# Kernel optimization log

Measured on AMD Instinct MI355X. Metric: run time of the kernel, lower is better.

The kernel has to match this reference:

```python
import jax, jax.numpy as jnp
import numpy as np
import math


def _forward(x, f0, theta, sigma, theta0, fbs, mix, w1, b1, w2, b2, conv_w):
    B, I, H, W = x.shape          # config requires B == I == H (== W here)
    S, O, _ = f0.shape            # config requires O == 1
    # ---- log-Gabor filter bank, fully vectorized over (scale, out, in) ----
    yy = jnp.linspace(-1.0, 1.0, H)[:, None]   # meshgrid 'ij': y along rows
    xx = jnp.linspace(-1.0, 1.0, W)[None, :]
    r = jnp.sqrt(xx ** 2 + yy ** 2 + 1e-6)     # [H,W]
    phi = jnp.arctan2(yy, xx)                  # [H,W]
    lr = jnp.log(r)
    log_gabor = jnp.exp(-(lr - jnp.log(f0)[..., None, None]) ** 2
                        / (2.0 * jnp.log(sigma)[..., None, None] ** 2))
    angular = jnp.exp(-(phi - theta[..., None, None]) ** 2
                      / (2.0 * theta0[..., None, None] ** 2))
    filters = log_gabor * angular              # [S,O,I,H,W]
    # ---- FFT (torch fftshift default shifts ALL dims; jnp matches) ----
    xs = jnp.fft.fftshift(jnp.fft.fft2(x))     # [B,I,H,W] complex64
    # ---- frequency attention (two 1x1 convs + softmax over scales) ----
    h1 = jax.nn.relu(jnp.einsum('bchw,oc->bohw', jnp.abs(xs), w1)
                     + b1[None, :, None, None])
    aw = jax.nn.softmax(jnp.einsum('bchw,sc->bshw', h1, w2)
                        + b2[None, :, None, None], axis=1)   # [B,S,H,W]
    # ---- attention-weighted combine. Faithful to torch broadcasting with
    # O==1 and B==I: attended[0,b,i,h,w] = sum_s xs[b,i]*F[s,0,i]*aw[i,s] ----
    attended = jnp.einsum('bihw,sihw,ishw->bihw', xs, filters[:, 0], aw)[None]
    # ---- dynamic frequency band mask (torch slices dims 2,3 = (Cin,H)) ----
    s_idx = jnp.floor((fbs[0, :, 0] + 1.0) / 2.0 * H).astype(jnp.int32)  # [I]
    e_idx = jnp.floor((fbs[0, :, 1] + 1.0) / 2.0 * H).astype(jnp.int32)
    arI = jnp.arange(I)
    arH = jnp.arange(H)
    mk = (arI[None, :] >= s_idx[:, None]) & (arI[None, :] < e_idx[:, None])  # [J,I]
    mh = (arH[None, :] >= s_idx[:, None]) & (arH[None, :] < e_idx[:, None])  # [J,H]
    mask = (mk[:, :, None] & mh[:, None, :]).astype(x.dtype)                 # [J,I,H]
    attended = attended * mask[None, :, :, :, None]
    # ---- back to spatial domain ----
    x_filtered = jnp.fft.ifft2(jnp.fft.ifftshift(attended)).real  # [1,B,I,H,W]
    # ---- spatial 3x3 conv path ----
    x_spatial = jax.lax.conv_general_dilated(
        x, conv_w, window_strides=(1, 1), padding=((1, 1), (1, 1)),
        dimension_numbers=('NCHW', 'OIHW', 'NCHW'))               # [B,1,H,W]
    return mix * x_filtered + (1.0 - mix) * x_spatial[None]


def setup_inputs() -> dict:
    key = jax.random.key(0)
    ks = jax.random.split(key, 10)
    B = I = H = W = 64
    O, S, HID = 1, 3, 64
    PI = math.pi
    x = jax.random.normal(ks[0], (B, I, H, W), dtype=jnp.float32)
    f0 = jnp.ones((S, O, I), jnp.float32)
    theta0 = jnp.ones((S, O, I), jnp.float32)
    sigma = jax.random.uniform(ks[1], (S, O, I), jnp.float32) * PI
    theta = jax.random.uniform(ks[2], (S, O, I), jnp.float32) * PI
    fbs = jax.random.uniform(ks[3], (O, I, 2), jnp.float32)
    mix = jax.random.uniform(ks[4], (1,), jnp.float32)
    w1 = jax.random.normal(ks[5], (HID, I), jnp.float32) * 0.05
    b1 = jnp.zeros((HID,), jnp.float32)
    w2 = jax.random.normal(ks[6], (S, HID), jnp.float32) * 0.05
    b2 = jnp.zeros((S,), jnp.float32)
    conv_w = jax.random.normal(ks[7], (O, I, 3, 3), jnp.float32) / math.sqrt(I * 9)
    return {'x': x, 'f0': f0, 'theta': theta, 'sigma': sigma, 'theta0': theta0,
            'fbs': fbs, 'mix': mix, 'w1': w1, 'b1': b1, 'w2': w2, 'b2': b2,
            'conv_w': conv_w}


def reference(x, f0, theta, sigma, theta0, fbs, mix, w1, b1, w2, b2, conv_w):
    return _forward(x, f0, theta, sigma, theta0, fbs, mix, w1, b1, w2, b2, conv_w)
```

## Files before the change

kernel.cpp:

```cpp
#include <hip/hip_runtime.h>

#define PI_D 3.14159265358979323846

namespace {
constexpr float CT[33] = {
  1.0000000000f,  0.9951847267f,  0.9807852804f,  0.9569403357f,
  0.9238795325f,  0.8819212643f,  0.8314696123f,  0.7730104534f,
  0.7071067812f,  0.6343932842f,  0.5555702330f,  0.4713967368f,
  0.3826834324f,  0.2902846773f,  0.1950903220f,  0.0980171403f,
  0.0f,          -0.0980171403f, -0.1950903220f, -0.2902846773f,
 -0.3826834324f, -0.4713967368f, -0.5555702330f, -0.6343932842f,
 -0.7071067812f, -0.7730104534f, -0.8314696123f, -0.8819212643f,
 -0.9238795325f, -0.9569403357f, -0.9807852804f, -0.9951847267f,
 -1.0f};
constexpr float STb[33] = {
  0.0f,           0.0980171403f,  0.1950903220f,  0.2902846773f,
  0.3826834324f,  0.4713967368f,  0.5555702330f,  0.6343932842f,
  0.7071067812f,  0.7730104534f,  0.8314696123f,  0.8819212643f,
  0.9238795325f,  0.9569403357f,  0.9807852804f,  0.9951847267f,
  1.0f,           0.9951847267f,  0.9807852804f,  0.9569403357f,
  0.9238795325f,  0.8819212643f,  0.8314696123f,  0.7730104534f,
  0.7071067812f,  0.6343932842f,  0.5555702330f,  0.4713967368f,
  0.3826834324f,  0.2902846773f,  0.1950903220f,  0.0980171403f,
  0.0f};
}

__device__ __forceinline__ void bitrev64(float v[64]) {
#pragma unroll
  for (int i = 0; i < 64; ++i) {
    const int j = (int)(__brev((unsigned)i) >> 26);
    if (j > i) { const float tv = v[i]; v[i] = v[j]; v[j] = tv; }
  }
}

template <bool INV, bool REAL>
__device__ __forceinline__ void fft64_stages(float re[64], float im[64]) {
#pragma unroll
  for (int s = 0; s < 6; ++s) {
    const int half = 1 << s;
    const int m = half << 1;
    const int tstep = 32 >> s;
#pragma unroll
    for (int k = 0; k < 64; k += m) {
#pragma unroll
      for (int j = 0; j < half; ++j) {
        const int ti = j * tstep;
        const int a = k + j, b = k + j + half;
        if (REAL && j == 0) {
          const float tr = re[b];
          re[b] = re[a] - tr;
          re[a] = re[a] + tr;
        } else if (REAL && ti == 16) {
          const float t0 = re[b];
          re[b] = re[a];
          im[b] = t0;
          im[a] = -t0;
        } else {
          float tr, tii;
          if (ti == 0) {
            tr = re[b]; tii = im[b];
          } else if (ti == 16) {
            if (INV) { tr = -im[b]; tii = re[b]; }
            else     { tr =  im[b]; tii = -re[b]; }
          } else {
            const float wr = CT[ti];
            const float wi = INV ? STb[ti] : -STb[ti];
            tr  = re[b] * wr - im[b] * wi;
            tii = re[b] * wi + im[b] * wr;
          }
          re[b] = re[a] - tr;  im[b] = im[a] - tii;
          re[a] = re[a] + tr;  im[a] = im[a] + tii;
        }
      }
    }
  }
}

template <bool INV>
__device__ __forceinline__ void fft64_regs(float re[64], float im[64]) {
  bitrev64(re);
  bitrev64(im);
  fft64_stages<INV, false>(re, im);
}

__device__ __forceinline__ void fft64_fwd_real(float re[64], float im[64]) {
  bitrev64(re);
  fft64_stages<false, true>(re, im);
}

__device__ __forceinline__ void band_from_fbs(const float* __restrict__ fbs,
                                              int c, int& s0, int& e0) {
  s0 = (int)floorf((fbs[2 * c]     + 1.0f) * 0.5f * 64.0f);
  e0 = (int)floorf((fbs[2 * c + 1] + 1.0f) * 0.5f * 64.0f);
}

__global__ __launch_bounds__(64) void k_fft_fwd(const float* __restrict__ x,
                                                float* __restrict__ F,
                                                const float* __restrict__ fbs,
                                                const float* __restrict__ w1,
                                                float* __restrict__ w1T) {
  __shared__ float buf[64][65];
  const int t = threadIdx.x;
  const int img = blockIdx.x;
  if (img == 0) {
    for (int k = 0; k < 64; ++k) w1T[t * 64 + k] = w1[k * 64 + t];
  }
  const float* xp = x + ((size_t)img << 12);
  const float4* xr4 = reinterpret_cast<const float4*>(xp + (t << 6));
  float re[64], im[64];
#pragma unroll
  for (int q = 0; q < 16; ++q) {
    const float4 v = xr4[q];
    re[4 * q]     = v.x; re[4 * q + 1] = v.y;
    re[4 * q + 2] = v.z; re[4 * q + 3] = v.w;
  }
#pragma unroll
  for (int j = 0; j < 64; ++j) im[j] = 0.0f;
  fft64_fwd_real(re, im);
#pragma unroll
  for (int j = 0; j < 64; ++j) buf[t][j] = re[j];
  __syncthreads();
#pragma unroll
  for (int j = 0; j < 64; ++j) re[j] = buf[j][t];
  __syncthreads();
#pragma unroll
  for (int j = 0; j < 64; ++j) buf[t][j] = im[j];
  __syncthreads();
#pragma unroll
  for (int j = 0; j < 64; ++j) im[j] = buf[j][t];
  fft64_regs<false>(re, im);
  const int b = img >> 6, i = img & 63;
  const int b_s = (b + 32) & 63, i_s = (i + 32) & 63;
  int s0, e0;
  band_from_fbs(fbs, b_s, s0, e0);
  float* Fre = F + ((size_t)img << 13);
  if ((i_s >= s0) && (i_s < e0)) {
    float* Fim = Fre + 4096;
#pragma unroll
    for (int j = 0; j < 64; ++j) {
      Fre[j * 64 + t] = re[j];
      Fim[j * 64 + t] = im[j];
    }
  } else {
#pragma unroll
    for (int j = 0; j < 64; ++j)
      Fre[j * 64 + t] = sqrtf(re[j] * re[j] + im[j] * im[j]);
  }
}

__global__ __launch_bounds__(64, 4) void k_attn_conv(
    const float* __restrict__ F, const float* __restrict__ w1T,
    const float* __restrict__ b1, const float* __restrict__ w2,
    const float* __restrict__ b2, const float* __restrict__ f0,
    const float* __restrict__ theta, const float* __restrict__ sigma,
    const float* __restrict__ theta0, const float* __restrict__ fbs,
    float* __restrict__ Wc,
    const float* __restrict__ x, const float* __restrict__ cw,
    const float* __restrict__ mixp, float* __restrict__ xsp,
    float* __restrict__ out) {
  const int t = threadIdx.x;
  const unsigned blk = blockIdx.x;
  const unsigned id = blk >> 1;

  if (blk & 1u) {
    const int lane = t;
    const int b = (int)(id >> 6);
    const int row = (int)(id & 63u);
    const float* xb = x + ((size_t)b << 18);
    const int rm = row > 0 ? row - 1 : 0;
    const int rp = row < 63 ? row + 1 : 63;
    float P00 = 0.f, P01 = 0.f, P02 = 0.f;
    float P10 = 0.f, P11 = 0.f, P12 = 0.f;
    float P20 = 0.f, P21 = 0.f, P22 = 0.f;
#pragma unroll 4
    for (int ch = 0; ch < 64; ++ch) {
      const float* xc = xb + (ch << 12);
      const float v0 = xc[(rm << 6) + lane];
      const float v1 = xc[(row << 6) + lane];
      const float v2 = xc[(rp << 6) + lane];
      const float* wp = cw + ch * 9;
      P00 = fmaf(v0, wp[0], P00);
      P01 = fmaf(v0, wp[1], P01);
      P02 = fmaf(v0, wp[2], P02);
      P10 = fmaf(v1, wp[3], P10);
      P11 = fmaf(v1, wp[4], P11);
      P12 = fmaf(v1, wp[5], P12);
      P20 = fmaf(v2, wp[6], P20);
      P21 = fmaf(v2, wp[7], P21);
      P22 = fmaf(v2, wp[8], P22);
    }
    const float tmask = (row > 0) ? 1.0f : 0.0f;
    const float bmask = (row < 63) ? 1.0f : 0.0f;
    const float Ql = tmask * P00 + P10 + bmask * P20;
    const float Qm = tmask * P01 + P11 + bmask * P21;
    const float Qr = tmask * P02 + P12 + bmask * P22;
    const float fromL = __shfl_up(Ql, 1, 64);
    const float fromR = __shfl_down(Qr, 1, 64);
    float acc = Qm;
    if (lane > 0) acc += fromL;
    if (lane < 63) acc += fromR;
    xsp[((size_t)b << 12) + (row << 6) + lane] = acc;
    const int b_s = (b + 32) & 63;
    int s0, e0;
    band_from_fbs(fbs, b_s, s0, e0);
    const float val = (1.0f - mixp[0]) * acc;
    float* ob = out + ((size_t)b << 18) + (row << 6) + lane;
#pragma unroll 4
    for (int i2 = 0; i2 < 64; ++i2) {
      const int i_s = (i2 + 32) & 63;
      if (!(i_s >= s0 && i_s < e0)) ob[(size_t)i2 << 12] = val;
    }
    return;
  }

  const int ai = (int)id;
  const int lane = t;
  const int i = ai >> 6;
  const int h = ai & 63;
  const int b_f = (i + 32) & 63;
  const int u_f = (h + 32) & 63;
  const int v_f = (lane + 32) & 63;
  const int pos_f = (u_f << 6) + v_f;
  int s0a, e0a;
  band_from_fbs(fbs, i, s0a, e0a);
  int alo = s0a < 0 ? 0 : (s0a > 64 ? 64 : s0a);
  int ahi = e0a < 0 ? 0 : (e0a > 64 ? 64 : e0a);
  if (ahi < alo) ahi = alo;
  float acc[64];
#pragma unroll
  for (int k = 0; k < 64; ++k) acc[k] = 0.0f;
  const float* Fb = F + ((size_t)(b_f << 6) << 13) + pos_f;
#pragma unroll 4
  for (int c = 0; c < alo; ++c) {
    const int c_f = (c + 32) & 63;
    const float mc = Fb[(size_t)c_f << 13];
    const float* wrow = w1T + (c << 6);
#pragma unroll
    for (int k = 0; k < 64; ++k) acc[k] = fmaf(wrow[k], mc, acc[k]);
  }
#pragma unroll 2
  for (int c = alo; c < ahi; ++c) {
    const int c_f = (c + 32) & 63;
    const float* base = Fb + ((size_t)c_f << 13);
    const float xr = base[0], xi = base[4096];
    const float mc = sqrtf(xr * xr + xi * xi);
    const float* wrow = w1T + (c << 6);
#pragma unroll
    for (int k = 0; k < 64; ++k) acc[k] = fmaf(wrow[k], mc, acc[k]);
  }
#pragma unroll 4
  for (int c = ahi; c < 64; ++c) {
    const int c_f = (c + 32) & 63;
    const float mc = Fb[(size_t)c_f << 13];
    const float* wrow = w1T + (c << 6);
#pragma unroll
    for (int k = 0; k < 64; ++k) acc[k] = fmaf(wrow[k], mc, acc[k]);
  }
  float l0 = b2[0], l1 = b2[1], l2 = b2[2];
#pragma unroll
  for (int k = 0; k < 64; ++k) {
    const float hv = fmaxf(acc[k] + b1[k], 0.0f);
    l0 = fmaf(w2[k], hv, l0);
    l1 = fmaf(w2[64 + k], hv, l1);
    l2 = fmaf(w2[128 + k], hv, l2);
  }
  float mx = fmaxf(l0, fmaxf(l1, l2));
  float e0v = expf(l0 - mx), e1 = expf(l1 - mx), e2 = expf(l2 - mx);
  float inv = 1.0f / (e0v + e1 + e2);
  float aw0 = e0v * inv, aw1 = e1 * inv, aw2 = e2 * inv;
  const float yy = -1.0f + (float)h * (2.0f / 63.0f);
  const float xx = -1.0f + (float)lane * (2.0f / 63.0f);
  const float r = sqrtf(xx * xx + yy * yy + 1e-6f);
  const float lr = logf(r);
  const float phi = atan2f(yy, xx);
  float wc = 0.0f;
  const float aws[3] = {aw0, aw1, aw2};
#pragma unroll
  for (int s = 0; s < 3; ++s) {
    const float f0v = f0[s * 64 + i];
    const float sgv = sigma[s * 64 + i];
    const float thv = theta[s * 64 + i];
    const float t0v = theta0[s * 64 + i];
    const float ls = logf(sgv);
    const float d1 = lr - logf(f0v);
    const float g1 = expf(-(d1 * d1) / (2.0f * ls * ls));
    const float d2 = phi - thv;
    const float g2 = expf(-(d2 * d2) / (2.0f * t0v * t0v));
    wc = fmaf(g1 * g2, aws[s], wc);
  }
  Wc[((i << 6) + h) * 64 + lane] = wc;
}

__global__ __launch_bounds__(64) void k_ifft_act(
    const float* __restrict__ F, const float* __restrict__ Wc,
    const float* __restrict__ xsp, const float* __restrict__ fbs,
    const float* __restrict__ mixp, float* __restrict__ out) {
  const int img = blockIdx.x;
  const int b = img >> 6, i = img & 63;
  const int b_s = (b + 32) & 63, i_s = (i + 32) & 63;
  int s0, e0;
  band_from_fbs(fbs, b_s, s0, e0);
  if (!((i_s >= s0) && (i_s < e0))) return;
  __shared__ float buf[64][65];
  const int t = threadIdx.x;
  const float* Fre = F + ((size_t)img << 13);
  const float* Fim = Fre + 4096;
  const float* Wcp = Wc + ((size_t)i_s << 12);
  const int u_s = (t + 32) & 63;
  const float rmask = (u_s >= s0 && u_s < e0) ? 1.0f : 0.0f;
  const float* wrow = Wcp + (u_s << 6);
  const float4* fr4 = reinterpret_cast<const float4*>(Fre + (t << 6));
  const float4* fi4 = reinterpret_cast<const float4*>(Fim + (t << 6));
  float re[64], im[64];
#pragma unroll
  for (int q = 0; q < 16; ++q) {
    const int j0 = 4 * q;
    const float4 w4 = *reinterpret_cast<const float4*>(wrow + ((j0 + 32) & 63));
    const float4 vr = fr4[q];
    const float4 vi = fi4[q];
    const float w0 = rmask * w4.x, w1v = rmask * w4.y;
    const float w2v = rmask * w4.z, w3v = rmask * w4.w;
    re[j0]     = vr.x * w0;  re[j0 + 1] = vr.y * w1v;
    re[j0 + 2] = vr.z * w2v; re[j0 + 3] = vr.w * w3v;
    im[j0]     = vi.x * w0;  im[j0 + 1] = vi.y * w1v;
    im[j0 + 2] = vi.z * w2v; im[j0 + 3] = vi.w * w3v;
  }
  fft64_regs<true>(re, im);
#pragma unroll
  for (int j = 0; j < 64; ++j) buf[t][j] = re[j];
  __syncthreads();
#pragma unroll
  for (int j = 0; j < 64; ++j) re[j] = buf[j][t];
  __syncthreads();
#pragma unroll
  for (int j = 0; j < 64; ++j) buf[t][j] = im[j];
  __syncthreads();
#pragma unroll
  for (int j = 0; j < 64; ++j) im[j] = buf[j][t];
  fft64_regs<true>(re, im);
  const float mixv = mixp[0];
  const float sc = mixv * (1.0f / 4096.0f);
  const float om = 1.0f - mixv;
  float* op = out + ((size_t)img << 12);
  const float* xp = xsp + ((size_t)b << 12);
#pragma unroll
  for (int j = 0; j < 64; ++j)
    op[j * 64 + t] = fmaf(sc, re[j], om * xp[j * 64 + t]);
}

extern "C" void kernel_launch(void* const* d_in, const int* in_sizes, int n_in,
                              void* d_out, int out_size, void* d_ws, size_t ws_size,
                              hipStream_t stream) {
  const float* x      = (const float*)d_in[0];
  const float* f0     = (const float*)d_in[1];
  const float* theta  = (const float*)d_in[2];
  const float* sigma  = (const float*)d_in[3];
  const float* theta0 = (const float*)d_in[4];
  const float* fbs    = (const float*)d_in[5];
  const float* mix    = (const float*)d_in[6];
  const float* w1     = (const float*)d_in[7];
  const float* b1     = (const float*)d_in[8];
  const float* w2     = (const float*)d_in[9];
  const float* b2     = (const float*)d_in[10];
  const float* cw     = (const float*)d_in[11];
  float* out = (float*)d_out;
  char* ws = (char*)d_ws;
  float* F   = (float*)(ws);
  float* Wc  = (float*)(ws + 134217728);
  float* xsp = (float*)(ws + 134217728 + 1048576);
  float* w1T = (float*)(ws + 134217728 + 2097152);

  k_fft_fwd<<<4096, 64, 0, stream>>>(x, F, fbs, w1, w1T);
  k_attn_conv<<<8192, 64, 0, stream>>>(F, w1T, b1, w2, b2, f0, theta, sigma,
                                       theta0, fbs, Wc, x, cw, mix, xsp, out);
  k_ifft_act<<<4096, 64, 0, stream>>>(F, Wc, xsp, fbs, mix, out);
}
```

Measured before the change: 234.0 us.

## Split attention hidden dimension across four waves with LDS reduction

The attention blocks grow to 256 threads, and each of the four waves computes 16 of the 64 hidden units. Partial logits are then reduced through shared memory, which cuts per-thread accumulator registers from 64 to 16 and should raise occupancy. The conv path now packs four rows per block, using a 4:1 block interleave instead of alternating blocks. The cost is a block barrier and redundant reads of F by all four waves, plus three idle waves after the reduction.

```diff
diff --git a/kernel.cpp b/kernel.cpp
--- a/kernel.cpp
+++ b/kernel.cpp
@@ -148,7 +148,7 @@
   }
 }
 
-__global__ __launch_bounds__(64, 4) void k_attn_conv(
+__global__ __launch_bounds__(256, 4) void k_attn_conv(
     const float* __restrict__ F, const float* __restrict__ w1T,
     const float* __restrict__ b1, const float* __restrict__ w2,
     const float* __restrict__ b2, const float* __restrict__ f0,
@@ -158,14 +158,17 @@
     const float* __restrict__ x, const float* __restrict__ cw,
     const float* __restrict__ mixp, float* __restrict__ xsp,
     float* __restrict__ out) {
+  __shared__ float part[4][3][64];
   const int t = threadIdx.x;
   const unsigned blk = blockIdx.x;
-  const unsigned id = blk >> 1;
-
-  if (blk & 1u) {
-    const int lane = t;
-    const int b = (int)(id >> 6);
-    const int row = (int)(id & 63u);
+  const unsigned q5 = blk / 5u;
+  const unsigned r5 = blk - q5 * 5u;
+
+  if (r5 == 4u) {
+    const int lane = t & 63;
+    const int cwv = t >> 6;
+    const int b = (int)(q5 >> 4);
+    const int row = (int)((q5 & 15u) << 2) | cwv;
     const float* xb = x + ((size_t)b << 18);
     const int rm = row > 0 ? row - 1 : 0;
     const int rp = row < 63 ? row + 1 : 63;
@@ -213,8 +216,10 @@
     return;
   }
 
-  const int ai = (int)id;
-  const int lane = t;
+  const int ai = (int)(4u * q5 + r5);
+  const int lane = t & 63;
+  const int wv = __builtin_amdgcn_readfirstlane(t >> 6);
+  const int k0 = wv << 4;
   const int i = ai >> 6;
   const int h = ai & 63;
   const int b_f = (i + 32) & 63;
@@ -226,17 +231,18 @@
   int alo = s0a < 0 ? 0 : (s0a > 64 ? 64 : s0a);
   int ahi = e0a < 0 ? 0 : (e0a > 64 ? 64 : e0a);
   if (ahi < alo) ahi = alo;
-  float acc[64];
-#pragma unroll
-  for (int k = 0; k < 64; ++k) acc[k] = 0.0f;
+  float acc[16];
+#pragma unroll
+  for (int k = 0; k < 16; ++k) acc[k] = 0.0f;
   const float* Fb = F + ((size_t)(b_f << 6) << 13) + pos_f;
+  const float* w1k = w1T + k0;
 #pragma unroll 4
   for (int c = 0; c < alo; ++c) {
     const int c_f = (c + 32) & 63;
     const float mc = Fb[(size_t)c_f << 13];
-    const float* wrow = w1T + (c << 6);
-#pragma unroll
-    for (int k = 0; k < 64; ++k) acc[k] = fmaf(wrow[k], mc, acc[k]);
+    const float* wrow = w1k + (c << 6);
+#pragma unroll
+    for (int k = 0; k < 16; ++k) acc[k] = fmaf(wrow[k], mc, acc[k]);
   }
 #pragma unroll 2
   for (int c = alo; c < ahi; ++c) {
@@ -244,26 +250,36 @@
     const float* base = Fb + ((size_t)c_f << 13);
     const float xr = base[0], xi = base[4096];
     const float mc = sqrtf(xr * xr + xi * xi);
-    const float* wrow = w1T + (c << 6);
-#pragma unroll
-    for (int k = 0; k < 64; ++k) acc[k] = fmaf(wrow[k], mc, acc[k]);
+    const float* wrow = w1k + (c << 6);
+#pragma unroll
+    for (int k = 0; k < 16; ++k) acc[k] = fmaf(wrow[k], mc, acc[k]);
   }
 #pragma unroll 4
   for (int c = ahi; c < 64; ++c) {
     const int c_f = (c + 32) & 63;
     const float mc = Fb[(size_t)c_f << 13];
-    const float* wrow = w1T + (c << 6);
-#pragma unroll
-    for (int k = 0; k < 64; ++k) acc[k] = fmaf(wrow[k], mc, acc[k]);
-  }
-  float l0 = b2[0], l1 = b2[1], l2 = b2[2];
-#pragma unroll
-  for (int k = 0; k < 64; ++k) {
-    const float hv = fmaxf(acc[k] + b1[k], 0.0f);
-    l0 = fmaf(w2[k], hv, l0);
-    l1 = fmaf(w2[64 + k], hv, l1);
-    l2 = fmaf(w2[128 + k], hv, l2);
-  }
+    const float* wrow = w1k + (c << 6);
+#pragma unroll
+    for (int k = 0; k < 16; ++k) acc[k] = fmaf(wrow[k], mc, acc[k]);
+  }
+  float p0 = 0.0f, p1 = 0.0f, p2 = 0.0f;
+#pragma unroll
+  for (int k = 0; k < 16; ++k) {
+    const float hv = fmaxf(acc[k] + b1[k0 + k], 0.0f);
+    p0 = fmaf(w2[k0 + k], hv, p0);
+    p1 = fmaf(w2[64 + k0 + k], hv, p1);
+    p2 = fmaf(w2[128 + k0 + k], hv, p2);
+  }
+  if (wv != 0) {
+    part[wv][0][lane] = p0;
+    part[wv][1][lane] = p1;
+    part[wv][2][lane] = p2;
+  }
+  __syncthreads();
+  if (wv != 0) return;
+  float l0 = b2[0] + p0 + part[1][0][lane] + part[2][0][lane] + part[3][0][lane];
+  float l1 = b2[1] + p1 + part[1][1][lane] + part[2][1][lane] + part[3][1][lane];
+  float l2 = b2[2] + p2 + part[1][2][lane] + part[2][2][lane] + part[3][2][lane];
   float mx = fmaxf(l0, fmaxf(l1, l2));
   float e0v = expf(l0 - mx), e1 = expf(l1 - mx), e2 = expf(l2 - mx);
   float inv = 1.0f / (e0v + e1 + e2);
@@ -371,7 +387,7 @@
   float* w1T = (float*)(ws + 134217728 + 2097152);
 
   k_fft_fwd<<<4096, 64, 0, stream>>>(x, F, fbs, w1, w1T);
-  k_attn_conv<<<8192, 64, 0, stream>>>(F, w1T, b1, w2, b2, f0, theta, sigma,
-                                       theta0, fbs, Wc, x, cw, mix, xsp, out);
+  k_attn_conv<<<5120, 256, 0, stream>>>(F, w1T, b1, w2, b2, f0, theta, sigma,
+                                        theta0, fbs, Wc, x, cw, mix, xsp, out);
   k_ifft_act<<<4096, 64, 0, stream>>>(F, Wc, xsp, fbs, mix, out);
 }
```

Result: faster. 212.2 us (-9.3%).
